# Kernel tuning notes

Measured on AMD Instinct MI355X. Metric: run time of the kernel, lower is better.

The kernel has to match this reference:

```python
import jax, jax.numpy as jnp
import numpy as np
import math

H = 16
D_MODEL = 1024
D_K = D_MODEL // H


def setup_inputs() -> dict:
    key = jax.random.key(0)
    ks = jax.random.split(key, 11)
    B, S, D = 4, 2048, D_MODEL
    scale = 1.0 / math.sqrt(D)
    inp = {
        "query": jax.random.normal(ks[0], (B, S, D), jnp.float32),
        "key": jax.random.normal(ks[1], (B, S, D), jnp.float32),
        "value": jax.random.normal(ks[2], (B, S, D), jnp.float32),
        # four Linear(d_model, d_model) layers: Wq, Wk, Wv, Wo (weights stored [in, out])
        "Wq": jax.random.normal(ks[3], (D, D), jnp.float32) * scale,
        "bq": jnp.zeros((D,), jnp.float32),
        "Wk": jax.random.normal(ks[4], (D, D), jnp.float32) * scale,
        "bk": jnp.zeros((D,), jnp.float32),
        "Wv": jax.random.normal(ks[5], (D, D), jnp.float32) * scale,
        "bv": jnp.zeros((D,), jnp.float32),
        "Wo": jax.random.normal(ks[6], (D, D), jnp.float32) * scale,
        "bo": jnp.zeros((D,), jnp.float32),
    }
    return inp


def reference(query, key, value, Wq, bq, Wk, bk, Wv, bv, Wo, bo):
    B, S, D = query.shape
    # QKV projections, split into heads: [B, H, S, d_k]
    def proj(x, W, b):
        return (x @ W + b).reshape(B, -1, H, D_K).transpose(0, 2, 1, 3)

    q = proj(query, Wq, bq)
    k = proj(key, Wk, bk)
    v = proj(value, Wv, bv)

    # scaled dot-product attention (mask=None, dropout p=0 -> identity)
    scores = jnp.einsum("bhqd,bhkd->bhqk", q, k) / math.sqrt(D_K)
    p_attn = jax.nn.softmax(scores, axis=-1)
    x = jnp.einsum("bhqk,bhkd->bhqd", p_attn, v)

    # merge heads and output projection
    x = x.transpose(0, 2, 1, 3).reshape(B, -1, H * D_K)
    return x @ Wo + bo
```

## Files before the change

### kernel.cpp

```cpp
#include <hip/hip_runtime.h>


typedef unsigned short u16;
typedef unsigned int u32;
typedef __attribute__((ext_vector_type(8))) short bfx8;
typedef __attribute__((ext_vector_type(4))) float f32x4;
typedef __attribute__((ext_vector_type(4))) float fx4;
typedef __attribute__((ext_vector_type(8))) u16 u16x8;
typedef __attribute__((ext_vector_type(2))) u32 u32x2;

__device__ __forceinline__ u16 f2bf(float f) {
  union { float f; u32 u; } v; v.f = f;
  u32 u = v.u;
  u += 0x7fffu + ((u >> 16) & 1u);
  return (u16)(u >> 16);
}

__device__ __forceinline__ u32 cvtpk(float a, float b) {
  u32 r;
  asm("v_cvt_pk_bf16_f32 %0, %1, %2" : "=v"(r) : "v"(a), "v"(b));
  return r;
}

__device__ __forceinline__ void gl_lds16(const void* g, void* l) {
  __builtin_amdgcn_global_load_lds((const __attribute__((address_space(1))) void*)g,
                                   (__attribute__((address_space(3))) void*)l, 16, 0, 0);
}

__global__ void cvt_bf16_3(const float* __restrict__ s0, const float* __restrict__ s1,
                           const float* __restrict__ s2, u16* __restrict__ outBase, int n) {
  const int z = blockIdx.y;
  const float* in = z == 0 ? s0 : (z == 1 ? s1 : s2);
  u16* out = outBase + (size_t)z * (8192ull * 1024);
  int i = (blockIdx.x * 256 + threadIdx.x) * 8;
  if (i >= n) return;
  fx4 a = *(const fx4*)(in + i);
  fx4 b = *(const fx4*)(in + i + 4);
  u16x8 o;
  o[0] = f2bf(a[0]); o[1] = f2bf(a[1]); o[2] = f2bf(a[2]); o[3] = f2bf(a[3]);
  o[4] = f2bf(b[0]); o[5] = f2bf(b[1]); o[6] = f2bf(b[2]); o[7] = f2bf(b[3]);
  *(u16x8*)(out + i) = o;
}

__global__ void wtrans4(const float* __restrict__ W0, const float* __restrict__ W1,
                        const float* __restrict__ W2, const float* __restrict__ W3,
                        u16* __restrict__ WtBase) {
  __shared__ float tile[64][65];
  const int z = blockIdx.z;
  const float* W = z == 0 ? W0 : (z == 1 ? W1 : (z == 2 ? W2 : W3));
  u16* Wt = WtBase + (size_t)z * (1024ull * 1024);
  const int t = threadIdx.x;
  const int n0 = blockIdx.x << 6, k0 = blockIdx.y << 6;
  {
    int r = t >> 2, c = (t & 3) << 4;
    const float* src = W + (size_t)(k0 + r) * 1024 + n0 + c;
#pragma unroll
    for (int u = 0; u < 4; ++u) {
      fx4 v = *(const fx4*)(src + u * 4);
      tile[r][c + u * 4 + 0] = v[0];
      tile[r][c + u * 4 + 1] = v[1];
      tile[r][c + u * 4 + 2] = v[2];
      tile[r][c + u * 4 + 3] = v[3];
    }
  }
  __syncthreads();
  {
    int nn = t >> 2, j = t & 3;
    u16x8 o0, o1;
#pragma unroll
    for (int e = 0; e < 8; ++e) o0[e] = f2bf(tile[(j << 4) + e][nn]);
#pragma unroll
    for (int e = 0; e < 8; ++e) o1[e] = f2bf(tile[(j << 4) + 8 + e][nn]);
    u16* dst = Wt + (size_t)(n0 + nn) * 1024 + k0 + (j << 4);
    *(u16x8*)dst = o0;
    *(u16x8*)(dst + 8) = o1;
  }
}

__global__ void vtrans(const u16* __restrict__ V, u16* __restrict__ Vt) {
  __shared__ u16 tile[64][65];
  const int t = threadIdx.x;
  const int pair = blockIdx.y, s0 = blockIdx.x << 6;
  const u16* src = V + ((size_t)pair << 17);
  {
    int r = t >> 2, c = (t & 3) << 4;
    const u16* p = src + (size_t)(s0 + r) * 64 + c;
    u16x8 v0 = *(const u16x8*)p;
    u16x8 v1 = *(const u16x8*)(p + 8);
#pragma unroll
    for (int u = 0; u < 8; ++u) { tile[r][c + u] = v0[u]; tile[r][c + 8 + u] = v1[u]; }
  }
  __syncthreads();
  {
    int d = t >> 2, j = t & 3;
    u16x8 o0, o1;
#pragma unroll
    for (int e = 0; e < 8; ++e) o0[e] = tile[(j << 4) + e][d];
#pragma unroll
    for (int e = 0; e < 8; ++e) o1[e] = tile[(j << 4) + 8 + e][d];
    u16* dst = Vt + ((size_t)pair << 17) + (size_t)d * 2048 + s0 + (j << 4);
    *(u16x8*)dst = o0;
    *(u16x8*)(dst + 8) = o1;
  }
}

template <int OUT_MODE>
__device__ __forceinline__ void gemm_body(const u16* __restrict__ A, const u16* __restrict__ Bt,
                                          const float* __restrict__ bias, void* __restrict__ out,
                                          float scale, char* smem) {
  const int t = threadIdx.x;
  const int w = t >> 6, l = t & 63;
  const int lg = l >> 4, lr = l & 15;
  const int wr = w >> 1, wc = w & 1;
  const int m0 = blockIdx.y << 7;
  const int n0 = blockIdx.x << 7;

  f32x4 acc[4][4] = {};

  const int trow = t >> 3;
  const int scb = ((t & 7) << 4) ^ ((trow & 7) << 4);
  const char* gA = (const char*)A + (size_t)(m0 + trow) * 2048;
  const char* gB = (const char*)Bt + (size_t)(n0 + trow) * 2048;

#define GSTAGE(kt, buf)                                                        \
  do {                                                                         \
    _Pragma("unroll")                                                          \
    for (int i = 0; i < 4; ++i) {                                              \
      gl_lds16(gA + (size_t)i * 32 * 2048 + ((kt) << 7) + scb,                 \
               (buf) + (((i << 8) + (w << 6)) << 4));                          \
      gl_lds16(gB + (size_t)i * 32 * 2048 + ((kt) << 7) + scb,                 \
               (buf) + 16384 + (((i << 8) + (w << 6)) << 4));                  \
    }                                                                          \
  } while (0)

  GSTAGE(0, smem);
  __syncthreads();

  for (int kt = 0; kt < 16; ++kt) {
    char* sA = smem + ((kt & 1) << 15);
    char* sB = sA + 16384;
    if (kt < 15) GSTAGE(kt + 1, smem + (((kt + 1) & 1) << 15));

#pragma unroll
    for (int kk = 0; kk < 2; ++kk) {
      const int off = ((kk << 6) + (lg << 4)) ^ ((lr & 7) << 4);
      bfx8 av[4], bv[4];
#pragma unroll
      for (int fi = 0; fi < 4; ++fi)
        av[fi] = *(const bfx8*)(sA + ((wr << 6) + (fi << 4) + lr) * 128 + off);
#pragma unroll
      for (int fj = 0; fj < 4; ++fj)
        bv[fj] = *(const bfx8*)(sB + ((wc << 6) + (fj << 4) + lr) * 128 + off);
#pragma unroll
      for (int fi = 0; fi < 4; ++fi)
#pragma unroll
        for (int fj = 0; fj < 4; ++fj)
          acc[fi][fj] = __builtin_amdgcn_mfma_f32_16x16x32_bf16(av[fi], bv[fj], acc[fi][fj], 0, 0, 0);
    }
    __syncthreads();
  }
#undef GSTAGE

#pragma unroll
  for (int fj = 0; fj < 4; ++fj) {
    const int n = n0 + (wc << 6) + (fj << 4) + lr;
    const float bv = bias[n];
#pragma unroll
    for (int fi = 0; fi < 4; ++fi) {
#pragma unroll
      for (int r = 0; r < 4; ++r) {
        const int m = m0 + (wr << 6) + (fi << 4) + (lg << 2) + r;
        const float val = (acc[fi][fj][r] + bv) * scale;
        if constexpr (OUT_MODE == 0) {
          const int b = m >> 11, s = m & 2047, h = n >> 6, d = n & 63;
          ((u16*)out)[(((size_t)(b * 16 + h) * 2048 + s) << 6) + d] = f2bf(val);
        } else {
          ((float*)out)[((size_t)m << 10) + n] = val;
        }
      }
    }
  }
}

__global__ void __launch_bounds__(256, 2)
gemm_qkv(const u16* __restrict__ A0, const u16* __restrict__ Wt0,
         const float* __restrict__ bq, const float* __restrict__ bk,
         const float* __restrict__ bv, u16* __restrict__ out0) {
  __shared__ __align__(16) char smem[65536];
  const int z = blockIdx.z;
  const u16* A = A0 + (size_t)z * (8192ull * 1024);
  const u16* Bt = Wt0 + (size_t)z * (1024ull * 1024);
  const float* bias = z == 0 ? bq : (z == 1 ? bk : bv);
  u16* out = out0 + (size_t)z * (8192ull * 1024);
  const float scale = z == 0 ? 0.18033688011112042f : 1.0f;
  gemm_body<0>(A, Bt, bias, out, scale, smem);
}

__global__ void __launch_bounds__(256, 2)
gemm_o(const u16* __restrict__ A, const u16* __restrict__ Bt,
       const float* __restrict__ bias, float* __restrict__ out) {
  __shared__ __align__(16) char smem[65536];
  gemm_body<1>(A, Bt, bias, out, 1.0f, smem);
}

__global__ void __launch_bounds__(512, 4)
attn_fwd(const u16* __restrict__ Qg, const u16* __restrict__ Kg,
         const u16* __restrict__ Vtg, u16* __restrict__ Og) {
  __shared__ __align__(16) char smem[65536];
  const int t = threadIdx.x;
  const int w = t >> 6, l = t & 63;
  const int lg = l >> 4, lr = l & 15;

  const int id = blockIdx.x;
  const int xcd = id & 7, slot = id >> 3;
  const int pair = ((slot >> 3) << 3) + xcd;
  const int q0 = (slot & 7) << 8;

  const char* Qb = (const char*)Qg + ((size_t)pair << 18);
  const char* Kb = (const char*)Kg + ((size_t)pair << 18);
  const char* Vb = (const char*)Vtg + ((size_t)pair << 18);
  char* sPw = smem + 32768 + (w << 12);

  const int trow = t >> 3;
  const int scb = ((t & 7) << 4) ^ ((trow & 7) << 4);
  const int ldst = (w << 10);

  bfx8 qf[2][2];
#pragma unroll
  for (int fi = 0; fi < 2; ++fi)
#pragma unroll
    for (int kk = 0; kk < 2; ++kk)
      qf[fi][kk] = *(const bfx8*)(Qb + (size_t)(q0 + (w << 5) + (fi << 4) + lr) * 128 +
                                  (kk << 6) + (lg << 4));

  f32x4 accO[2][4] = {};
  float Lp[2] = {0.f, 0.f};
  const int sw0 = (lr & 7) << 4;

#define ASTAGE(kt, buf)                                                         \
  do {                                                                          \
    gl_lds16(Kb + (size_t)(kt) * 8192 + (size_t)trow * 128 + scb, (buf) + ldst);\
    gl_lds16(Vb + (size_t)trow * 4096 + (size_t)(kt) * 128 + scb,               \
             (buf) + 8192 + ldst);                                              \
  } while (0)

  ASTAGE(0, smem);
  __syncthreads();

  for (int it = 0; it < 32; ++it) {
    char* bK = smem + ((it & 1) << 14);
    char* bV = bK + 8192;
    if (it < 31) ASTAGE(it + 1, smem + (((it + 1) & 1) << 14));

    f32x4 accS[2][4] = {};
    __builtin_amdgcn_s_setprio(1);
#pragma unroll
    for (int kk = 0; kk < 2; ++kk) {
      const int off = ((kk << 6) + (lg << 4)) ^ sw0;
      bfx8 kf[4];
#pragma unroll
      for (int fj = 0; fj < 4; ++fj)
        kf[fj] = *(const bfx8*)(bK + (((fj << 4) + lr) << 7) + off);
#pragma unroll
      for (int fi = 0; fi < 2; ++fi)
#pragma unroll
        for (int fj = 0; fj < 4; ++fj)
          accS[fi][fj] = __builtin_amdgcn_mfma_f32_16x16x32_bf16(kf[fj], qf[fi][kk], accS[fi][fj], 0, 0, 0);
    }
    __builtin_amdgcn_s_setprio(0);

#pragma unroll
    for (int fi = 0; fi < 2; ++fi) {
      char* prow = sPw + (((fi << 4) + lr) << 7);
#pragma unroll
      for (int fj = 0; fj < 4; ++fj) {
        const float p0 = __builtin_amdgcn_exp2f(accS[fi][fj][0]);
        const float p1 = __builtin_amdgcn_exp2f(accS[fi][fj][1]);
        const float p2 = __builtin_amdgcn_exp2f(accS[fi][fj][2]);
        const float p3 = __builtin_amdgcn_exp2f(accS[fi][fj][3]);
        Lp[fi] += (p0 + p1) + (p2 + p3);
        u32x2 pk;
        pk[0] = cvtpk(p0, p1);
        pk[1] = cvtpk(p2, p3);
        *(u32x2*)(prow + (((fj << 5) + (lg << 3)) ^ sw0)) = pk;
      }
    }

    __builtin_amdgcn_s_setprio(1);
#pragma unroll
    for (int kk = 0; kk < 2; ++kk) {
      const int off = ((kk << 6) + (lg << 4)) ^ sw0;
      bfx8 pf[2], vf[4];
#pragma unroll
      for (int fi = 0; fi < 2; ++fi)
        pf[fi] = *(const bfx8*)(sPw + (((fi << 4) + lr) << 7) + off);
#pragma unroll
      for (int dj = 0; dj < 4; ++dj)
        vf[dj] = *(const bfx8*)(bV + (((dj << 4) + lr) << 7) + off);
#pragma unroll
      for (int fi = 0; fi < 2; ++fi)
#pragma unroll
        for (int dj = 0; dj < 4; ++dj)
          accO[fi][dj] = __builtin_amdgcn_mfma_f32_16x16x32_bf16(pf[fi], vf[dj], accO[fi][dj], 0, 0, 0);
    }
    __builtin_amdgcn_s_setprio(0);

    __syncthreads();
  }
#undef ASTAGE

  __builtin_amdgcn_sched_barrier(0);
  float* Lbuf = (float*)sPw;
#pragma unroll
  for (int fi = 0; fi < 2; ++fi)
    Lbuf[(lg << 5) + (fi << 4) + lr] = Lp[fi];

  float rinv[2][4];
#pragma unroll
  for (int fi = 0; fi < 2; ++fi)
#pragma unroll
    for (int r = 0; r < 4; ++r) {
      const int qrow = (fi << 4) + (lg << 2) + r;
      float s = Lbuf[qrow] + Lbuf[32 + qrow] + Lbuf[64 + qrow] + Lbuf[96 + qrow];
      rinv[fi][r] = 1.0f / s;
    }
  __builtin_amdgcn_sched_barrier(0);

  const int b = pair >> 4, h = pair & 15;
#pragma unroll
  for (int fi = 0; fi < 2; ++fi) {
    u16* bb = (u16*)sPw;
#pragma unroll
    for (int dj = 0; dj < 4; ++dj)
#pragma unroll
      for (int r = 0; r < 4; ++r)
        bb[((lg << 2) + r) * 72 + (dj << 4) + lr] = f2bf(accO[fi][dj][r] * rinv[fi][r]);

    const int rrow = l >> 2, rc = (l & 3) << 4;
    u16x8 o0 = *(const u16x8*)(bb + rrow * 72 + rc);
    u16x8 o1 = *(const u16x8*)(bb + rrow * 72 + rc + 8);
    const int srow = q0 + (w << 5) + (fi << 4) + rrow;
    u16* dst = Og + (((size_t)(b * 2048 + srow)) << 10) + (h << 6) + rc;
    *(u16x8*)dst = o0;
    *(u16x8*)(dst + 8) = o1;
  }
}

extern "C" void kernel_launch(void* const* d_in, const int* in_sizes, int n_in,
                              void* d_out, int out_size, void* d_ws, size_t ws_size,
                              hipStream_t stream) {
  const float* q  = (const float*)d_in[0];
  const float* k  = (const float*)d_in[1];
  const float* v  = (const float*)d_in[2];
  const float* Wq = (const float*)d_in[3];
  const float* bq = (const float*)d_in[4];
  const float* Wk = (const float*)d_in[5];
  const float* bk = (const float*)d_in[6];
  const float* Wv = (const float*)d_in[7];
  const float* bv = (const float*)d_in[8];
  const float* Wo = (const float*)d_in[9];
  const float* bo = (const float*)d_in[10];
  float* out = (float*)d_out;
  char* ws = (char*)d_ws;

  const size_t MB = 1024 * 1024;
  if (ws_size < 104 * MB) return;

  u16* inq = (u16*)(ws + 0 * MB);
  u16* wqt = (u16*)(ws + 48 * MB);
  u16* wot = (u16*)(ws + 54 * MB);
  u16* Qh  = (u16*)(ws + 56 * MB);
  u16* Vh  = (u16*)(ws + 88 * MB);
  u16* Vth = (u16*)(ws + 16 * MB);
  u16* Ob  = inq;

  const int NTOK = 8192 * 1024;
  cvt_bf16_3<<<dim3(4096, 3), 256, 0, stream>>>(q, k, v, inq, NTOK);
  wtrans4<<<dim3(16, 16, 4), 256, 0, stream>>>(Wq, Wk, Wv, Wo, wqt);
  gemm_qkv<<<dim3(8, 64, 3), 256, 0, stream>>>(inq, wqt, bq, bk, bv, Qh);
  vtrans<<<dim3(32, 64), 256, 0, stream>>>(Vh, Vth);
  attn_fwd<<<512, 512, 0, stream>>>(Qh, (const u16*)(ws + 72 * MB), Vth, Ob);
  gemm_o<<<dim3(8, 64), 256, 0, stream>>>(Ob, wot, bo, out);
}
```

Baseline: 204.7 us.

## Use 256x256 QKV GEMM with ping-pong pipeline and fuse V transpose

Replaces the 128x128 QKV projection GEMM with a 256x256-tile, 512-thread kernel. It double-buffers global-to-LDS loads, uses a swizzled LDS layout, interleaves barriers, and raises wave priority around MFMA phases. The V projection epilogue writes directly in transposed [d][s] layout with packed 4-element stores, removing the separate vtrans kernel and its extra pass over V. The costs are higher register pressure from the 8x4 accumulators and a grid of only 384 blocks, which may underfill the GPU.

```diff
diff --git a/kernel.cpp b/kernel.cpp
--- a/kernel.cpp
+++ b/kernel.cpp
@@ -7,6 +7,7 @@
 typedef __attribute__((ext_vector_type(4))) float f32x4;
 typedef __attribute__((ext_vector_type(4))) float fx4;
 typedef __attribute__((ext_vector_type(8))) u16 u16x8;
+typedef __attribute__((ext_vector_type(4))) u16 u16x4;
 typedef __attribute__((ext_vector_type(2))) u32 u32x2;
 
 __device__ __forceinline__ u16 f2bf(float f) {
@@ -77,37 +78,134 @@
   }
 }
 
-__global__ void vtrans(const u16* __restrict__ V, u16* __restrict__ Vt) {
-  __shared__ u16 tile[64][65];
+__global__ void __launch_bounds__(512, 2)
+gemm_qkv8(const u16* __restrict__ A0, const u16* __restrict__ Wt0,
+          const float* __restrict__ bq, const float* __restrict__ bk,
+          const float* __restrict__ bv, u16* __restrict__ out0, u16* __restrict__ vt) {
+  __shared__ __align__(16) char smem[65536];
   const int t = threadIdx.x;
-  const int pair = blockIdx.y, s0 = blockIdx.x << 6;
-  const u16* src = V + ((size_t)pair << 17);
-  {
-    int r = t >> 2, c = (t & 3) << 4;
-    const u16* p = src + (size_t)(s0 + r) * 64 + c;
-    u16x8 v0 = *(const u16x8*)p;
-    u16x8 v1 = *(const u16x8*)(p + 8);
-#pragma unroll
-    for (int u = 0; u < 8; ++u) { tile[r][c + u] = v0[u]; tile[r][c + 8 + u] = v1[u]; }
-  }
-  __syncthreads();
-  {
-    int d = t >> 2, j = t & 3;
-    u16x8 o0, o1;
-#pragma unroll
-    for (int e = 0; e < 8; ++e) o0[e] = tile[(j << 4) + e][d];
-#pragma unroll
-    for (int e = 0; e < 8; ++e) o1[e] = tile[(j << 4) + 8 + e][d];
-    u16* dst = Vt + ((size_t)pair << 17) + (size_t)d * 2048 + s0 + (j << 4);
-    *(u16x8*)dst = o0;
-    *(u16x8*)(dst + 8) = o1;
-  }
-}
-
-template <int OUT_MODE>
-__device__ __forceinline__ void gemm_body(const u16* __restrict__ A, const u16* __restrict__ Bt,
-                                          const float* __restrict__ bias, void* __restrict__ out,
-                                          float scale, char* smem) {
+  const int w = t >> 6, l = t & 63;
+  const int lg = l >> 4, lr = l & 15;
+  const int wr = w >> 2, wc = w & 3;
+  const int z = blockIdx.z;
+  const int n0 = blockIdx.x << 8;
+  const int m0 = blockIdx.y << 8;
+
+  const u16* A = A0 + (size_t)z * (8192ull * 1024);
+  const u16* Bt = Wt0 + (size_t)z * (1024ull * 1024);
+  const float* bias = z == 0 ? bq : (z == 1 ? bk : bv);
+  const float scale = z == 0 ? 0.18033688011112042f : 1.0f;
+
+  const int q_ = (t & 7) ^ ((t >> 3) & 7);
+  const int rowL0 = 2 * (t >> 3) + (q_ >> 2);
+  const int colb = (q_ & 3) << 4;
+  const char* gA0 = (const char*)A + (size_t)(m0 + rowL0) * 2048 + colb;
+  const char* gA1 = (const char*)A + (size_t)(m0 + rowL0 + 128) * 2048 + colb;
+  const char* gB0 = (const char*)Bt + (size_t)(n0 + rowL0) * 2048 + colb;
+  const char* gB1 = (const char*)Bt + (size_t)(n0 + rowL0 + 128) * 2048 + colb;
+
+#define QSTAGE(kt, bufb)                                                      \
+  do {                                                                        \
+    gl_lds16(gA0 + (size_t)(kt) * 64, (bufb) + (w << 10));                    \
+    gl_lds16(gA1 + (size_t)(kt) * 64, (bufb) + 8192 + (w << 10));             \
+    gl_lds16(gB0 + (size_t)(kt) * 64, (bufb) + 16384 + (w << 10));            \
+    gl_lds16(gB1 + (size_t)(kt) * 64, (bufb) + 24576 + (w << 10));            \
+  } while (0)
+
+  const int slot = (((lr & 1) << 2) + lg) ^ ((lr >> 1) & 7);
+  const int aoff = ((wr << 6) + (lr >> 1)) * 128 + (slot << 4);
+  const int boff = 16384 + ((wc << 5) + (lr >> 1)) * 128 + (slot << 4);
+
+  f32x4 acc[8][4] = {};
+
+  QSTAGE(0, smem);
+  QSTAGE(1, smem + 32768);
+  asm volatile("s_waitcnt vmcnt(4)" ::: "memory");
+  __builtin_amdgcn_sched_barrier(0);
+  __builtin_amdgcn_s_barrier();
+
+#pragma unroll 2
+  for (int kt = 0; kt < 32; ++kt) {
+    const int p = kt & 1;
+    const char* pA = smem + (p << 15) + aoff;
+    const char* pB = smem + (p << 15) + boff;
+
+    bfx8 av[4], bv4[4];
+#pragma unroll
+    for (int m = 0; m < 4; ++m) av[m] = *(const bfx8*)(pA + m * 1024);
+#pragma unroll
+    for (int n = 0; n < 4; ++n) bv4[n] = *(const bfx8*)(pB + n * 1024);
+    __builtin_amdgcn_s_barrier();
+    __builtin_amdgcn_s_setprio(1);
+#pragma unroll
+    for (int m = 0; m < 4; ++m)
+#pragma unroll
+      for (int n = 0; n < 4; ++n)
+        acc[m][n] = __builtin_amdgcn_mfma_f32_16x16x32_bf16(av[m], bv4[n], acc[m][n], 0, 0, 0);
+    __builtin_amdgcn_s_setprio(0);
+    __builtin_amdgcn_s_barrier();
+
+    bfx8 av2[4];
+#pragma unroll
+    for (int m = 0; m < 4; ++m) av2[m] = *(const bfx8*)(pA + (4 + m) * 1024);
+    asm volatile("s_waitcnt lgkmcnt(0)" ::: "memory");
+    __builtin_amdgcn_sched_barrier(0);
+    __builtin_amdgcn_s_barrier();
+    if (kt < 30) QSTAGE(kt + 2, smem + (p << 15));
+    __builtin_amdgcn_s_setprio(1);
+#pragma unroll
+    for (int m = 0; m < 4; ++m)
+#pragma unroll
+      for (int n = 0; n < 4; ++n)
+        acc[4 + m][n] = __builtin_amdgcn_mfma_f32_16x16x32_bf16(av2[m], bv4[n], acc[4 + m][n], 0, 0, 0);
+    __builtin_amdgcn_s_setprio(0);
+    if (kt < 30) { asm volatile("s_waitcnt vmcnt(4)" ::: "memory"); }
+    else         { asm volatile("s_waitcnt vmcnt(0)" ::: "memory"); }
+    __builtin_amdgcn_sched_barrier(0);
+    __builtin_amdgcn_s_barrier();
+  }
+#undef QSTAGE
+
+  if (z < 2) {
+#pragma unroll
+    for (int n = 0; n < 4; ++n) {
+      const int nn = n0 + (wc << 6) + (n << 4) + lr;
+      const float bvl = bias[nn];
+      const int h = nn >> 6, d = nn & 63;
+#pragma unroll
+      for (int m = 0; m < 8; ++m) {
+#pragma unroll
+        for (int r = 0; r < 4; ++r) {
+          const int mm = m0 + (wr << 7) + (m << 4) + (lg << 2) + r;
+          const int b = mm >> 11, s = mm & 2047;
+          out0[(size_t)z * (8192ull * 1024) +
+               (((size_t)(b * 16 + h) * 2048 + s) << 6) + d] = f2bf((acc[m][n][r] + bvl) * scale);
+        }
+      }
+    }
+  } else {
+#pragma unroll
+    for (int n = 0; n < 4; ++n) {
+      const int nn = n0 + (wc << 6) + (n << 4) + lr;
+      const float bvl = bias[nn];
+      const int h = nn >> 6, d = nn & 63;
+#pragma unroll
+      for (int m = 0; m < 8; ++m) {
+        const int mm = m0 + (wr << 7) + (m << 4) + (lg << 2);
+        const int b = mm >> 11, s = mm & 2047;
+        u16x4 pk4;
+#pragma unroll
+        for (int r = 0; r < 4; ++r) pk4[r] = f2bf(acc[m][n][r] + bvl);
+        *(u16x4*)(vt + (size_t)(b * 16 + h) * 131072 + (size_t)d * 2048 + s) = pk4;
+      }
+    }
+  }
+}
+
+__global__ void __launch_bounds__(256, 2)
+gemm_o(const u16* __restrict__ A, const u16* __restrict__ Bt,
+       const float* __restrict__ bias, float* __restrict__ out) {
+  __shared__ __align__(16) char smem[65536];
   const int t = threadIdx.x;
   const int w = t >> 6, l = t & 63;
   const int lg = l >> 4, lr = l & 15;
@@ -164,43 +262,16 @@
 #pragma unroll
   for (int fj = 0; fj < 4; ++fj) {
     const int n = n0 + (wc << 6) + (fj << 4) + lr;
-    const float bv = bias[n];
+    const float bvl = bias[n];
 #pragma unroll
     for (int fi = 0; fi < 4; ++fi) {
 #pragma unroll
       for (int r = 0; r < 4; ++r) {
         const int m = m0 + (wr << 6) + (fi << 4) + (lg << 2) + r;
-        const float val = (acc[fi][fj][r] + bv) * scale;
-        if constexpr (OUT_MODE == 0) {
-          const int b = m >> 11, s = m & 2047, h = n >> 6, d = n & 63;
-          ((u16*)out)[(((size_t)(b * 16 + h) * 2048 + s) << 6) + d] = f2bf(val);
-        } else {
-          ((float*)out)[((size_t)m << 10) + n] = val;
-        }
+        out[((size_t)m << 10) + n] = acc[fi][fj][r] + bvl;
       }
     }
   }
-}
-
-__global__ void __launch_bounds__(256, 2)
-gemm_qkv(const u16* __restrict__ A0, const u16* __restrict__ Wt0,
-         const float* __restrict__ bq, const float* __restrict__ bk,
-         const float* __restrict__ bv, u16* __restrict__ out0) {
-  __shared__ __align__(16) char smem[65536];
-  const int z = blockIdx.z;
-  const u16* A = A0 + (size_t)z * (8192ull * 1024);
-  const u16* Bt = Wt0 + (size_t)z * (1024ull * 1024);
-  const float* bias = z == 0 ? bq : (z == 1 ? bk : bv);
-  u16* out = out0 + (size_t)z * (8192ull * 1024);
-  const float scale = z == 0 ? 0.18033688011112042f : 1.0f;
-  gemm_body<0>(A, Bt, bias, out, scale, smem);
-}
-
-__global__ void __launch_bounds__(256, 2)
-gemm_o(const u16* __restrict__ A, const u16* __restrict__ Bt,
-       const float* __restrict__ bias, float* __restrict__ out) {
-  __shared__ __align__(16) char smem[65536];
-  gemm_body<1>(A, Bt, bias, out, 1.0f, smem);
 }
 
 __global__ void __launch_bounds__(512, 4)
@@ -370,15 +441,14 @@
   u16* wqt = (u16*)(ws + 48 * MB);
   u16* wot = (u16*)(ws + 54 * MB);
   u16* Qh  = (u16*)(ws + 56 * MB);
-  u16* Vh  = (u16*)(ws + 88 * MB);
-  u16* Vth = (u16*)(ws + 16 * MB);
+  u16* Kh  = (u16*)(ws + 72 * MB);
+  u16* Vth = (u16*)(ws + 88 * MB);
   u16* Ob  = inq;
 
   const int NTOK = 8192 * 1024;
   cvt_bf16_3<<<dim3(4096, 3), 256, 0, stream>>>(q, k, v, inq, NTOK);
   wtrans4<<<dim3(16, 16, 4), 256, 0, stream>>>(Wq, Wk, Wv, Wo, wqt);
-  gemm_qkv<<<dim3(8, 64, 3), 256, 0, stream>>>(inq, wqt, bq, bk, bv, Qh);
-  vtrans<<<dim3(32, 64), 256, 0, stream>>>(Vh, Vth);
-  attn_fwd<<<512, 512, 0, stream>>>(Qh, (const u16*)(ws + 72 * MB), Vth, Ob);
+  gemm_qkv8<<<dim3(4, 32, 3), 512, 0, stream>>>(inq, wqt, bq, bk, bv, Qh, Vth);
+  attn_fwd<<<512, 512, 0, stream>>>(Qh, Kh, Vth, Ob);
   gemm_o<<<dim3(8, 64), 256, 0, stream>>>(Ob, wot, bo, out);
 }
```

Measured after the change: 209.3 us. +2.3%, slower.

## Fuse V transpose into QKV GEMM epilogue, merge prep kernels, remap GEMM tiles per XCD

Applied to the files above, without the earlier changes.

The V projection epilogue now writes the transposed [pair, d, s] layout directly as packed 4-element stores. This removes the separate vtrans kernel and its extra round trip through global memory. The input-conversion and weight-transpose kernels are merged into a single launch. The GEMM block-to-tile mapping is remapped so that blocks sharing a B column land on the same XCD, aiming for better L2 reuse. The risk is strided, less coalesced stores in the V epilogue.

```diff
diff --git a/kernel.cpp b/kernel.cpp
--- a/kernel.cpp
+++ b/kernel.cpp
@@ -7,6 +7,7 @@
 typedef __attribute__((ext_vector_type(4))) float f32x4;
 typedef __attribute__((ext_vector_type(4))) float fx4;
 typedef __attribute__((ext_vector_type(8))) u16 u16x8;
+typedef __attribute__((ext_vector_type(4))) u16 u16x4;
 typedef __attribute__((ext_vector_type(2))) u32 u32x2;
 
 __device__ __forceinline__ u16 f2bf(float f) {
@@ -27,93 +28,66 @@
                                    (__attribute__((address_space(3))) void*)l, 16, 0, 0);
 }
 
-__global__ void cvt_bf16_3(const float* __restrict__ s0, const float* __restrict__ s1,
-                           const float* __restrict__ s2, u16* __restrict__ outBase, int n) {
-  const int z = blockIdx.y;
-  const float* in = z == 0 ? s0 : (z == 1 ? s1 : s2);
-  u16* out = outBase + (size_t)z * (8192ull * 1024);
-  int i = (blockIdx.x * 256 + threadIdx.x) * 8;
-  if (i >= n) return;
-  fx4 a = *(const fx4*)(in + i);
-  fx4 b = *(const fx4*)(in + i + 4);
-  u16x8 o;
-  o[0] = f2bf(a[0]); o[1] = f2bf(a[1]); o[2] = f2bf(a[2]); o[3] = f2bf(a[3]);
-  o[4] = f2bf(b[0]); o[5] = f2bf(b[1]); o[6] = f2bf(b[2]); o[7] = f2bf(b[3]);
-  *(u16x8*)(out + i) = o;
-}
-
-__global__ void wtrans4(const float* __restrict__ W0, const float* __restrict__ W1,
-                        const float* __restrict__ W2, const float* __restrict__ W3,
-                        u16* __restrict__ WtBase) {
+__global__ void prep(const float* __restrict__ q, const float* __restrict__ k,
+                     const float* __restrict__ v, u16* __restrict__ inBase,
+                     const float* __restrict__ W0, const float* __restrict__ W1,
+                     const float* __restrict__ W2, const float* __restrict__ W3,
+                     u16* __restrict__ WtBase) {
   __shared__ float tile[64][65];
-  const int z = blockIdx.z;
-  const float* W = z == 0 ? W0 : (z == 1 ? W1 : (z == 2 ? W2 : W3));
-  u16* Wt = WtBase + (size_t)z * (1024ull * 1024);
+  const int bid = blockIdx.x;
   const int t = threadIdx.x;
-  const int n0 = blockIdx.x << 6, k0 = blockIdx.y << 6;
-  {
-    int r = t >> 2, c = (t & 3) << 4;
-    const float* src = W + (size_t)(k0 + r) * 1024 + n0 + c;
-#pragma unroll
-    for (int u = 0; u < 4; ++u) {
-      fx4 v = *(const fx4*)(src + u * 4);
-      tile[r][c + u * 4 + 0] = v[0];
-      tile[r][c + u * 4 + 1] = v[1];
-      tile[r][c + u * 4 + 2] = v[2];
-      tile[r][c + u * 4 + 3] = v[3];
-    }
-  }
-  __syncthreads();
-  {
-    int nn = t >> 2, j = t & 3;
-    u16x8 o0, o1;
-#pragma unroll
-    for (int e = 0; e < 8; ++e) o0[e] = f2bf(tile[(j << 4) + e][nn]);
-#pragma unroll
-    for (int e = 0; e < 8; ++e) o1[e] = f2bf(tile[(j << 4) + 8 + e][nn]);
-    u16* dst = Wt + (size_t)(n0 + nn) * 1024 + k0 + (j << 4);
-    *(u16x8*)dst = o0;
-    *(u16x8*)(dst + 8) = o1;
-  }
-}
-
-__global__ void vtrans(const u16* __restrict__ V, u16* __restrict__ Vt) {
-  __shared__ u16 tile[64][65];
-  const int t = threadIdx.x;
-  const int pair = blockIdx.y, s0 = blockIdx.x << 6;
-  const u16* src = V + ((size_t)pair << 17);
-  {
-    int r = t >> 2, c = (t & 3) << 4;
-    const u16* p = src + (size_t)(s0 + r) * 64 + c;
-    u16x8 v0 = *(const u16x8*)p;
-    u16x8 v1 = *(const u16x8*)(p + 8);
-#pragma unroll
-    for (int u = 0; u < 8; ++u) { tile[r][c + u] = v0[u]; tile[r][c + 8 + u] = v1[u]; }
-  }
-  __syncthreads();
-  {
-    int d = t >> 2, j = t & 3;
-    u16x8 o0, o1;
-#pragma unroll
-    for (int e = 0; e < 8; ++e) o0[e] = tile[(j << 4) + e][d];
-#pragma unroll
-    for (int e = 0; e < 8; ++e) o1[e] = tile[(j << 4) + 8 + e][d];
-    u16* dst = Vt + ((size_t)pair << 17) + (size_t)d * 2048 + s0 + (j << 4);
-    *(u16x8*)dst = o0;
-    *(u16x8*)(dst + 8) = o1;
-  }
-}
-
-template <int OUT_MODE>
+  if (bid < 12288) {
+    const int z = bid >> 12, xb = bid & 4095;
+    const float* in = z == 0 ? q : (z == 1 ? k : v);
+    u16* out = inBase + (size_t)z * (8192ull * 1024);
+    const int i = (xb * 256 + t) * 8;
+    fx4 a = *(const fx4*)(in + i);
+    fx4 b = *(const fx4*)(in + i + 4);
+    u16x8 o;
+    o[0] = f2bf(a[0]); o[1] = f2bf(a[1]); o[2] = f2bf(a[2]); o[3] = f2bf(a[3]);
+    o[4] = f2bf(b[0]); o[5] = f2bf(b[1]); o[6] = f2bf(b[2]); o[7] = f2bf(b[3]);
+    *(u16x8*)(out + i) = o;
+  } else {
+    const int wb = bid - 12288;
+    const int z = wb >> 8, rem = wb & 255;
+    const float* W = z == 0 ? W0 : (z == 1 ? W1 : (z == 2 ? W2 : W3));
+    u16* Wt = WtBase + (size_t)z * (1024ull * 1024);
+    const int n0 = (rem & 15) << 6, k0 = (rem >> 4) << 6;
+    {
+      int r = t >> 2, c = (t & 3) << 4;
+      const float* src = W + (size_t)(k0 + r) * 1024 + n0 + c;
+#pragma unroll
+      for (int u = 0; u < 4; ++u) {
+        fx4 vv = *(const fx4*)(src + u * 4);
+        tile[r][c + u * 4 + 0] = vv[0];
+        tile[r][c + u * 4 + 1] = vv[1];
+        tile[r][c + u * 4 + 2] = vv[2];
+        tile[r][c + u * 4 + 3] = vv[3];
+      }
+    }
+    __syncthreads();
+    {
+      int nn = t >> 2, j = t & 3;
+      u16x8 o0, o1;
+#pragma unroll
+      for (int e = 0; e < 8; ++e) o0[e] = f2bf(tile[(j << 4) + e][nn]);
+#pragma unroll
+      for (int e = 0; e < 8; ++e) o1[e] = f2bf(tile[(j << 4) + 8 + e][nn]);
+      u16* dst = Wt + (size_t)(n0 + nn) * 1024 + k0 + (j << 4);
+      *(u16x8*)dst = o0;
+      *(u16x8*)(dst + 8) = o1;
+    }
+  }
+}
+
+template <int EPI>
 __device__ __forceinline__ void gemm_body(const u16* __restrict__ A, const u16* __restrict__ Bt,
                                           const float* __restrict__ bias, void* __restrict__ out,
-                                          float scale, char* smem) {
+                                          float scale, char* smem, int m0, int n0) {
   const int t = threadIdx.x;
   const int w = t >> 6, l = t & 63;
   const int lg = l >> 4, lr = l & 15;
   const int wr = w >> 1, wc = w & 1;
-  const int m0 = blockIdx.y << 7;
-  const int n0 = blockIdx.x << 7;
 
   f32x4 acc[4][4] = {};
 
@@ -164,43 +138,67 @@
 #pragma unroll
   for (int fj = 0; fj < 4; ++fj) {
     const int n = n0 + (wc << 6) + (fj << 4) + lr;
-    const float bv = bias[n];
+    const float bvl = bias[n];
 #pragma unroll
     for (int fi = 0; fi < 4; ++fi) {
-#pragma unroll
-      for (int r = 0; r < 4; ++r) {
-        const int m = m0 + (wr << 6) + (fi << 4) + (lg << 2) + r;
-        const float val = (acc[fi][fj][r] + bv) * scale;
-        if constexpr (OUT_MODE == 0) {
-          const int b = m >> 11, s = m & 2047, h = n >> 6, d = n & 63;
-          ((u16*)out)[(((size_t)(b * 16 + h) * 2048 + s) << 6) + d] = f2bf(val);
-        } else {
-          ((float*)out)[((size_t)m << 10) + n] = val;
+      if constexpr (EPI == 2) {
+        const int h = n >> 6, d = n & 63;
+        const int mm = m0 + (wr << 6) + (fi << 4) + (lg << 2);
+        const int b = mm >> 11, s = mm & 2047;
+        u16x4 pk4;
+#pragma unroll
+        for (int r = 0; r < 4; ++r) pk4[r] = f2bf(acc[fi][fj][r] + bvl);
+        *(u16x4*)((u16*)out + (size_t)(b * 16 + h) * 131072 + (size_t)d * 2048 + s) = pk4;
+      } else {
+#pragma unroll
+        for (int r = 0; r < 4; ++r) {
+          const int m = m0 + (wr << 6) + (fi << 4) + (lg << 2) + r;
+          const float val = (acc[fi][fj][r] + bvl) * scale;
+          if constexpr (EPI == 0) {
+            const int b = m >> 11, s = m & 2047, h = n >> 6, d = n & 63;
+            ((u16*)out)[(((size_t)(b * 16 + h) * 2048 + s) << 6) + d] = f2bf(val);
+          } else {
+            ((float*)out)[((size_t)m << 10) + n] = val;
+          }
         }
       }
     }
   }
+}
+
+__device__ __forceinline__ void xcd_remap(int& m0, int& n0) {
+  const int lin = blockIdx.x + (blockIdx.y << 3);
+  const int c = lin & 7, j = lin >> 3;
+  m0 = (((j & 7) << 3) + c) << 7;
+  n0 = (j >> 3) << 7;
 }
 
 __global__ void __launch_bounds__(256, 2)
 gemm_qkv(const u16* __restrict__ A0, const u16* __restrict__ Wt0,
          const float* __restrict__ bq, const float* __restrict__ bk,
-         const float* __restrict__ bv, u16* __restrict__ out0) {
+         const float* __restrict__ bv, u16* __restrict__ out0, u16* __restrict__ vt) {
   __shared__ __align__(16) char smem[65536];
   const int z = blockIdx.z;
+  int m0, n0;
+  xcd_remap(m0, n0);
   const u16* A = A0 + (size_t)z * (8192ull * 1024);
   const u16* Bt = Wt0 + (size_t)z * (1024ull * 1024);
-  const float* bias = z == 0 ? bq : (z == 1 ? bk : bv);
-  u16* out = out0 + (size_t)z * (8192ull * 1024);
-  const float scale = z == 0 ? 0.18033688011112042f : 1.0f;
-  gemm_body<0>(A, Bt, bias, out, scale, smem);
+  if (z == 2) {
+    gemm_body<2>(A, Bt, bv, vt, 1.0f, smem, m0, n0);
+  } else {
+    const float* bias = z == 0 ? bq : bk;
+    const float scale = z == 0 ? 0.18033688011112042f : 1.0f;
+    gemm_body<0>(A, Bt, bias, out0 + (size_t)z * (8192ull * 1024), scale, smem, m0, n0);
+  }
 }
 
 __global__ void __launch_bounds__(256, 2)
 gemm_o(const u16* __restrict__ A, const u16* __restrict__ Bt,
        const float* __restrict__ bias, float* __restrict__ out) {
   __shared__ __align__(16) char smem[65536];
-  gemm_body<1>(A, Bt, bias, out, 1.0f, smem);
+  int m0, n0;
+  xcd_remap(m0, n0);
+  gemm_body<1>(A, Bt, bias, out, 1.0f, smem, m0, n0);
 }
 
 __global__ void __launch_bounds__(512, 4)
@@ -370,15 +368,12 @@
   u16* wqt = (u16*)(ws + 48 * MB);
   u16* wot = (u16*)(ws + 54 * MB);
   u16* Qh  = (u16*)(ws + 56 * MB);
-  u16* Vh  = (u16*)(ws + 88 * MB);
-  u16* Vth = (u16*)(ws + 16 * MB);
+  u16* Kh  = (u16*)(ws + 72 * MB);
+  u16* Vth = (u16*)(ws + 88 * MB);
   u16* Ob  = inq;
 
-  const int NTOK = 8192 * 1024;
-  cvt_bf16_3<<<dim3(4096, 3), 256, 0, stream>>>(q, k, v, inq, NTOK);
-  wtrans4<<<dim3(16, 16, 4), 256, 0, stream>>>(Wq, Wk, Wv, Wo, wqt);
-  gemm_qkv<<<dim3(8, 64, 3), 256, 0, stream>>>(inq, wqt, bq, bk, bv, Qh);
-  vtrans<<<dim3(32, 64), 256, 0, stream>>>(Vh, Vth);
-  attn_fwd<<<512, 512, 0, stream>>>(Qh, (const u16*)(ws + 72 * MB), Vth, Ob);
+  prep<<<13312, 256, 0, stream>>>(q, k, v, inq, Wq, Wk, Wv, Wo, wqt);
+  gemm_qkv<<<dim3(8, 64, 3), 256, 0, stream>>>(inq, wqt, bq, bk, bv, Qh, Vth);
+  attn_fwd<<<512, 512, 0, stream>>>(Qh, Kh, Vth, Ob);
   gemm_o<<<dim3(8, 64), 256, 0, stream>>>(Ob, wot, bo, out);
 }
```

Result: faster. 186.9 us (-8.7%).
